# Optimization experiments

Hardware: AMD Instinct MI355X
Metric: run time of the kernel (lower is better)

The kernel has to match this reference:

```python
import jax, jax.numpy as jnp
import numpy as np

S = 3          # number of atomic species (experts)
N = 20000      # total atoms
F = 1920       # soap_size = S*(S+1)/2 * max_radial^2 * (max_angular+1) = 6*64*5
H = 512        # num_neurons_per_layer
NSTRUCT = 16   # number of structures (systems)
EPS = 1e-5


def setup_inputs() -> dict:
    key = jax.random.key(0)
    ks = jax.random.split(key, 12)
    std = 0.02
    return {
        "features": jax.random.normal(ks[0], (N, F), jnp.float32),
        "ln_gamma": jnp.ones((S, F), jnp.float32) + std * jax.random.normal(ks[1], (S, F), jnp.float32),
        "ln_beta": std * jax.random.normal(ks[2], (S, F), jnp.float32),
        "W1": std * jax.random.normal(ks[3], (S, F, H), jnp.float32),
        "b1": std * jax.random.normal(ks[4], (S, H), jnp.float32),
        "W2": std * jax.random.normal(ks[5], (S, H, H), jnp.float32),
        "b2": std * jax.random.normal(ks[6], (S, H), jnp.float32),
        "w3": std * jax.random.normal(ks[7], (S, H), jnp.float32),
        "b3": std * jax.random.normal(ks[8], (S,), jnp.float32),
        "comp_w": jax.random.normal(ks[9], (S,), jnp.float32),
        "species": jax.random.randint(ks[10], (N,), 0, S, dtype=jnp.int32),
        "struct_id": jax.random.randint(ks[11], (N,), 0, NSTRUCT, dtype=jnp.int32),
    }


def _silu(x):
    return x * jax.nn.sigmoid(x)


def reference(features, ln_gamma, ln_beta, W1, b1, W2, b2, w3, b3, comp_w, species, struct_id):
    # Per-species LayerNorm (LayerNormMap): normalization is species-independent,
    # only the affine params differ, so gather them per atom.
    mu = jnp.mean(features, axis=-1, keepdims=True)
    var = jnp.var(features, axis=-1, keepdims=True)
    xhat = (features - mu) * jax.lax.rsqrt(var + EPS)
    xln = xhat * ln_gamma[species] + ln_beta[species]  # [N, F]

    # Hard-routed per-species MLP (MLPMap) + per-species Linear->1 (LinearMap).
    # Small fixed loop over S experts; each atom keeps the output of its own expert.
    e = jnp.zeros((features.shape[0],), features.dtype)
    for s in range(S):
        h = _silu(xln @ W1[s] + b1[s])       # [N, H]
        h = _silu(h @ W2[s] + b2[s])         # [N, H]
        es = h @ w3[s] + b3[s]               # [N]
        e = jnp.where(species == s, es, e)

    # apply_composition_contribution: add per-species composition weight
    e = e + comp_w[species]

    # sum_over_samples(['atom','center_type']): per-structure energy
    energy = jax.ops.segment_sum(e, struct_id, num_segments=NSTRUCT)  # [NSTRUCT]
    return energy
```

## Files before the change

kernel.cpp:

```cpp
#include <hip/hip_runtime.h>
#include <cstdint>
#include <cstddef>

#define N_ATOMS 20000
#define F_DIM 1920
#define H_DIM 512
#define S_NUM 3
#define NSTRUCT_ 16
#define MAXT64 315
#define NCNT 8

#define QW 846.6667f
#define STEP_W (0.15f / 127.f)
#define QH 16.0f
#define STEP_H (1.f / 16.f)

typedef __bf16 bf16;
typedef float f32x4 __attribute__((ext_vector_type(4)));
typedef int i32x4 __attribute__((ext_vector_type(4)));

__device__ __forceinline__ void gload_lds16(const void* g, void* l) {
  __builtin_amdgcn_global_load_lds(
      (const __attribute__((address_space(1))) unsigned int*)g,
      (__attribute__((address_space(3))) unsigned int*)l, 16, 0, 0);
}

#define CNT8_OFF 16

__global__ __launch_bounds__(256) void prep_kernel(const float* __restrict__ W1,
                                                   int8_t* __restrict__ W1T,
                                                   const float* __restrict__ W2,
                                                   int8_t* __restrict__ W2T,
                                                   const int* __restrict__ species,
                                                   int* ints, float* out) {
  int id = blockIdx.x;
  if (id >= 912) {
    int cb = id - 912;
    int tid = threadIdx.x;
    if (cb == 0) {
      if (tid < 3) ints[tid] = 0;
      if (tid < NSTRUCT_) out[tid] = 0.f;
    }
    int base = cb * (N_ATOMS / NCNT);
    int end = base + (N_ATOMS / NCNT);
    int c0 = 0, c1 = 0, c2 = 0;
    for (int i = base + tid; i < end; i += 256) {
      int s = species[i];
      c0 += (s == 0);
      c1 += (s == 1);
      c2 += (s == 2);
    }
#pragma unroll
    for (int m = 1; m < 64; m <<= 1) {
      c0 += __shfl_xor(c0, m);
      c1 += __shfl_xor(c1, m);
      c2 += __shfl_xor(c2, m);
    }
    __shared__ int red[4][3];
    if ((tid & 63) == 0) {
      red[tid >> 6][0] = c0;
      red[tid >> 6][1] = c1;
      red[tid >> 6][2] = c2;
    }
    __syncthreads();
    if (tid == 0) {
      int* slot = ints + CNT8_OFF + cb * 3;
      slot[0] = red[0][0] + red[1][0] + red[2][0] + red[3][0];
      slot[1] = red[0][1] + red[1][1] + red[2][1] + red[3][1];
      slot[2] = red[0][2] + red[1][2] + red[2][2] + red[3][2];
    }
    return;
  }
  __shared__ float tile[64][65];
  const float* ins;
  int8_t* outs;
  int R, C, r0, c0;
  if (id < 720) {
    int sp = id / 240, rem = id % 240;
    R = F_DIM;
    C = H_DIM;
    c0 = (rem & 7) * 64;
    r0 = (rem >> 3) * 64;
    ins = W1 + (size_t)sp * R * C;
    outs = W1T + (size_t)sp * R * C;
  } else {
    int id2 = id - 720;
    int sp = id2 / 64, rem = id2 % 64;
    R = H_DIM;
    C = H_DIM;
    c0 = (rem & 7) * 64;
    r0 = (rem >> 3) * 64;
    ins = W2 + (size_t)sp * R * C;
    outs = W2T + (size_t)sp * R * C;
  }
  int tc = threadIdx.x & 63, tr4 = threadIdx.x >> 6;
#pragma unroll
  for (int it = 0; it < 16; ++it) {
    int r = it * 4 + tr4;
    tile[r][tc] = ins[(size_t)(r0 + r) * C + c0 + tc];
  }
  __syncthreads();
#pragma unroll
  for (int it = 0; it < 16; ++it) {
    int oc = it * 4 + tr4;
    float q = fminf(fmaxf(rintf(tile[tc][oc] * QW), -127.f), 127.f);
    outs[(size_t)(c0 + oc) * R + r0 + tc] = (int8_t)(int)q;
  }
}


__global__ void scatter_kernel(const int* __restrict__ species, int* ints,
                               int* idx_list, int* pos_of) {
  int n0 = 0, n1 = 0, n2 = 0;
#pragma unroll
  for (int b = 0; b < NCNT; ++b) {
    const int* slot = ints + CNT8_OFF + b * 3;
    n0 += slot[0];
    n1 += slot[1];
    n2 += slot[2];
  }
  int offs_l[4] = {0, n0, n0 + n1, N_ATOMS};
  if (blockIdx.x == 0 && threadIdx.x == 0) {
    int* offs = ints + 6;
    int* toffs = ints + 10;
    offs[0] = 0;
    offs[1] = n0;
    offs[2] = n0 + n1;
    offs[3] = N_ATOMS;
    int t0 = (n0 + 63) >> 6, t1 = (n1 + 63) >> 6, t2 = (n2 + 63) >> 6;
    toffs[0] = 0;
    toffs[1] = t0;
    toffs[2] = t0 + t1;
    toffs[3] = t0 + t1 + t2;
  }
  int* pos = ints;
  int i = blockIdx.x * 256 + threadIdx.x;
  int lane = threadIdx.x & 63;
  int sp = (i < N_ATOMS) ? species[i] : -1;
#pragma unroll
  for (int s = 0; s < S_NUM; ++s) {
    unsigned long long mask = __ballot(sp == s);
    if (!mask) continue;
    int leader = __ffsll((long long)mask) - 1;
    int base = 0;
    if (lane == leader) base = atomicAdd(&pos[s], __popcll(mask));
    base = __shfl(base, leader);
    if (sp == s) {
      int rank = __popcll(mask & ((1ULL << lane) - 1ULL));
      int p = offs_l[s] + base + rank;
      idx_list[p] = i;
      pos_of[i] = p;
    }
  }
}


__global__ __launch_bounds__(256) void ln_kernel(
    const float* __restrict__ feat, const float* __restrict__ gamma,
    const float* __restrict__ beta, const int* __restrict__ species,
    const int* __restrict__ pos_of, int8_t* __restrict__ xq,
    float* __restrict__ srowA) {
  int atom = blockIdx.x, tid = threadIdx.x;
  const float4* frow = (const float4*)(feat + (size_t)atom * F_DIM);
  float4 v0 = frow[tid];
  bool has2 = tid < 224;
  float4 v1 = has2 ? frow[256 + tid] : make_float4(0.f, 0.f, 0.f, 0.f);
  float s = v0.x + v0.y + v0.z + v0.w;
  float s2 = v0.x * v0.x + v0.y * v0.y + v0.z * v0.z + v0.w * v0.w;
  if (has2) {
    s += v1.x + v1.y + v1.z + v1.w;
    s2 += v1.x * v1.x + v1.y * v1.y + v1.z * v1.z + v1.w * v1.w;
  }
#pragma unroll
  for (int m = 1; m < 64; m <<= 1) {
    s += __shfl_xor(s, m);
    s2 += __shfl_xor(s2, m);
  }
  __shared__ float red[4][2];
  __shared__ float redm[4];
  if ((tid & 63) == 0) { red[tid >> 6][0] = s; red[tid >> 6][1] = s2; }
  __syncthreads();
  s = red[0][0] + red[1][0] + red[2][0] + red[3][0];
  s2 = red[0][1] + red[1][1] + red[2][1] + red[3][1];
  float mu = s * (1.f / F_DIM);
  float var = s2 * (1.f / F_DIM) - mu * mu;
  float rsig = rsqrtf(var + 1e-5f);
  int sp = species[atom];
  size_t p = (size_t)pos_of[atom];
  const float4* g4 = (const float4*)(gamma + (size_t)sp * F_DIM);
  const float4* b4 = (const float4*)(beta + (size_t)sp * F_DIM);
  float o0[4], o1[4];
  {
    float4 g = g4[tid], b = b4[tid];
    o0[0] = (v0.x - mu) * rsig * g.x + b.x;
    o0[1] = (v0.y - mu) * rsig * g.y + b.y;
    o0[2] = (v0.z - mu) * rsig * g.z + b.z;
    o0[3] = (v0.w - mu) * rsig * g.w + b.w;
  }
  if (has2) {
    float4 g = g4[256 + tid], b = b4[256 + tid];
    o1[0] = (v1.x - mu) * rsig * g.x + b.x;
    o1[1] = (v1.y - mu) * rsig * g.y + b.y;
    o1[2] = (v1.z - mu) * rsig * g.z + b.z;
    o1[3] = (v1.w - mu) * rsig * g.w + b.w;
  } else {
    o1[0] = o1[1] = o1[2] = o1[3] = 0.f;
  }
  float am = fmaxf(fmaxf(fabsf(o0[0]), fabsf(o0[1])), fmaxf(fabsf(o0[2]), fabsf(o0[3])));
  am = fmaxf(am, fmaxf(fmaxf(fabsf(o1[0]), fabsf(o1[1])), fmaxf(fabsf(o1[2]), fabsf(o1[3]))));
#pragma unroll
  for (int m = 1; m < 64; m <<= 1) am = fmaxf(am, __shfl_xor(am, m));
  if ((tid & 63) == 0) redm[tid >> 6] = am;
  __syncthreads();
  am = fmaxf(fmaxf(redm[0], redm[1]), fmaxf(redm[2], redm[3]));
  am = fmaxf(am, 1e-8f);
  float qs = 127.f / am;
  if (tid == 0) srowA[p] = am * (1.f / 127.f);
  unsigned int* orow = (unsigned int*)(xq + p * F_DIM);
  {
    int q0 = (int)rintf(o0[0] * qs), q1 = (int)rintf(o0[1] * qs);
    int q2 = (int)rintf(o0[2] * qs), q3 = (int)rintf(o0[3] * qs);
    orow[tid] = (q0 & 255) | ((q1 & 255) << 8) | ((q2 & 255) << 16) | ((q3 & 255) << 24);
  }
  if (has2) {
    int q0 = (int)rintf(o1[0] * qs), q1 = (int)rintf(o1[1] * qs);
    int q2 = (int)rintf(o1[2] * qs), q3 = (int)rintf(o1[3] * qs);
    orow[256 + tid] = (q0 & 255) | ((q1 & 255) << 8) | ((q2 & 255) << 16) | ((q3 & 255) << 24);
  }
}


template <int EPI>
__global__ __launch_bounds__(64, 2) void gemm_kernel(
    const int8_t* __restrict__ A, int lda_e, const int8_t* __restrict__ BT, int K,
    const float* __restrict__ bias, const float* __restrict__ w3,
    const float* __restrict__ srowA, int8_t* __restrict__ Hout,
    float* __restrict__ e_part, const int* __restrict__ ints) {
  __shared__ char smem[24576];
  const int* offs = ints + 6;
  const int* toffs = ints + 10;

  int total = gridDim.x;
  int lid = blockIdx.x;
  int q = total >> 3, r = total & 7;
  int xcd = lid & 7, sl = lid >> 3;
  int w = (xcd < r ? xcd * (q + 1) : r * (q + 1) + (xcd - r) * q) + sl;
  int bx = w & 3;
  int t = w >> 2;
  if (t >= toffs[3]) return;
  int sp = (t >= toffs[1]) + (t >= toffs[2]);
  int by = t - toffs[sp];

  int rstart = offs[sp], rend = offs[sp + 1];
  int r0 = rstart + by * 64;

  int lane = threadIdx.x;
  int n0 = bx * 128;

  const char* Ag = (const char*)A;
  size_t ldab = (size_t)lda_e;
  const char* Bg = (const char*)(BT + (size_t)sp * H_DIM * K);
  size_t ldbb = (size_t)K;

  int l8 = lane >> 3;
  int sw_st = (((lane & 7) ^ l8) << 4);

  auto stage = [&](int kt) {
    int k0b = kt * 128;
#pragma unroll
    for (int c = 0; c < 8; ++c) {
      int row = c * 8 + l8;
      int ar = r0 + row;
      if (ar > rend - 1) ar = rend - 1;
      gload_lds16(Ag + (size_t)ar * ldab + k0b + sw_st, &smem[c * 1024]);
    }
#pragma unroll
    for (int c = 0; c < 16; ++c) {
      int row = c * 8 + l8;
      gload_lds16(Bg + (size_t)(n0 + row) * ldbb + k0b + sw_st, &smem[8192 + c * 1024]);
    }
  };

  i32x4 acc[4][8];
#pragma unroll
  for (int a_ = 0; a_ < 4; ++a_)
#pragma unroll
    for (int b_ = 0; b_ < 8; ++b_) {
      i32x4 z = {0, 0, 0, 0};
      acc[a_][b_] = z;
    }

  int lr = lane & 15, lg = lane >> 4;
  int swr = (lr & 7) << 4;

  auto compute = [&]() {
#pragma unroll
    for (int kh = 0; kh < 2; ++kh) {
      int off = (kh * 64 + lg * 16) ^ swr;
      i32x4 av[4], bv[8];
#pragma unroll
      for (int fm = 0; fm < 4; ++fm)
        av[fm] = *(const i32x4*)(&smem[(fm * 16 + lr) * 128 + off]);
#pragma unroll
      for (int fn = 0; fn < 8; ++fn)
        bv[fn] = *(const i32x4*)(&smem[8192 + (fn * 16 + lr) * 128 + off]);
#pragma unroll
      for (int fm = 0; fm < 4; ++fm)
#pragma unroll
        for (int fn = 0; fn < 8; ++fn)
          acc[fm][fn] =
              __builtin_amdgcn_mfma_i32_16x16x64_i8(av[fm], bv[fn], acc[fm][fn], 0, 0, 0);
    }
  };

  int NT = K / 128;
#pragma unroll 1
  for (int kt = 0; kt < NT; ++kt) {
    stage(kt);
    __syncthreads();
    compute();
    __syncthreads();
  }

  const float* bs = bias + sp * H_DIM;
  if (EPI == 0) {
#pragma unroll
    for (int fm = 0; fm < 4; ++fm)
#pragma unroll
      for (int i = 0; i < 4; ++i) {
        int rr = r0 + fm * 16 + lg * 4 + i;
        if (rr < rend) {
          float deq = srowA[rr] * STEP_W;
#pragma unroll
          for (int fn = 0; fn < 8; ++fn) {
            int c = n0 + fn * 16 + lr;
            float x = (float)acc[fm][fn][i] * deq + bs[c];
            float h = x / (1.f + __expf(-x));
            float qh = fminf(fmaxf(rintf(h * QH), -127.f), 127.f);
            Hout[(size_t)rr * H_DIM + c] = (int8_t)(int)qh;
          }
        }
      }
  } else {
    const float* ws3 = w3 + sp * H_DIM;
    float* ep = e_part + (size_t)bx * N_ATOMS;
    const float deq = STEP_H * STEP_W;
#pragma unroll
    for (int fm = 0; fm < 4; ++fm)
#pragma unroll
      for (int i = 0; i < 4; ++i) {
        int rr = r0 + fm * 16 + lg * 4 + i;
        float part = 0.f;
#pragma unroll
        for (int fn = 0; fn < 8; ++fn) {
          int c = n0 + fn * 16 + lr;
          float x = (float)acc[fm][fn][i] * deq + bs[c];
          part += (x / (1.f + __expf(-x))) * ws3[c];
        }
        part += __shfl_xor(part, 1);
        part += __shfl_xor(part, 2);
        part += __shfl_xor(part, 4);
        part += __shfl_xor(part, 8);
        if (lr == 0 && rr < rend) ep[rr] = part;
      }
  }
}


__global__ void finalize_kernel(const float* __restrict__ e_part, const int* __restrict__ ints,
                                const float* __restrict__ b3, const float* __restrict__ comp_w,
                                const int* __restrict__ idx_list,
                                const int* __restrict__ struct_id, float* out) {
  const int* offs = ints + 6;
  __shared__ float bins[NSTRUCT_];
  if (threadIdx.x < NSTRUCT_) bins[threadIdx.x] = 0.f;
  __syncthreads();
  int rr = blockIdx.x * 256 + threadIdx.x;
  if (rr < N_ATOMS) {
    float e = 0.f;
#pragma unroll
    for (int p = 0; p < 4; ++p) e += e_part[(size_t)p * N_ATOMS + rr];
    int s = (rr >= offs[1]) + (rr >= offs[2]);
    e += b3[s] + comp_w[s];
    atomicAdd(&bins[struct_id[idx_list[rr]]], e);
  }
  __syncthreads();
  if (threadIdx.x < NSTRUCT_) atomicAdd(&out[threadIdx.x], bins[threadIdx.x]);
}


extern "C" void kernel_launch(void* const* d_in, const int* in_sizes, int n_in,
                              void* d_out, int out_size, void* d_ws, size_t ws_size,
                              hipStream_t stream) {
  const float* features = (const float*)d_in[0];
  const float* ln_gamma = (const float*)d_in[1];
  const float* ln_beta = (const float*)d_in[2];
  const float* W1 = (const float*)d_in[3];
  const float* b1 = (const float*)d_in[4];
  const float* W2 = (const float*)d_in[5];
  const float* b2 = (const float*)d_in[6];
  const float* w3 = (const float*)d_in[7];
  const float* b3 = (const float*)d_in[8];
  const float* comp_w = (const float*)d_in[9];
  const int* species = (const int*)d_in[10];
  const int* struct_id = (const int*)d_in[11];
  float* out = (float*)d_out;

  char* ws = (char*)d_ws;
  size_t off = 0;
  auto alloc = [&](size_t bytes) {
    char* p = ws + off;
    off += (bytes + 255) & ~(size_t)255;
    return p;
  };
  int8_t* W1T = (int8_t*)alloc((size_t)S_NUM * H_DIM * F_DIM);
  int8_t* W2T = (int8_t*)alloc((size_t)S_NUM * H_DIM * H_DIM);
  int8_t* xq = (int8_t*)alloc((size_t)N_ATOMS * F_DIM);
  int8_t* h1q = (int8_t*)alloc((size_t)N_ATOMS * H_DIM);
  float* srowA = (float*)alloc((size_t)N_ATOMS * 4);
  float* e_part = (float*)alloc((size_t)4 * N_ATOMS * 4);
  int* idx_list = (int*)alloc((size_t)N_ATOMS * 4);
  int* pos_of = (int*)alloc((size_t)N_ATOMS * 4);
  int* ints = (int*)alloc(256);

  int nb = (N_ATOMS + 255) / 256;
  prep_kernel<<<912 + NCNT, 256, 0, stream>>>(W1, W1T, W2, W2T, species, ints, out);
  scatter_kernel<<<nb, 256, 0, stream>>>(species, ints, idx_list, pos_of);
  ln_kernel<<<N_ATOMS, 256, 0, stream>>>(features, ln_gamma, ln_beta, species, pos_of, xq,
                                         srowA);

  gemm_kernel<0><<<4 * MAXT64, 64, 0, stream>>>(xq, F_DIM, W1T, F_DIM, b1, nullptr, srowA,
                                                h1q, nullptr, ints);
  gemm_kernel<1><<<4 * MAXT64, 64, 0, stream>>>(h1q, H_DIM, W2T, H_DIM, b2, w3, nullptr,
                                                nullptr, e_part, ints);
  finalize_kernel<<<nb, 256, 0, stream>>>(e_part, ints, b3, comp_w, idx_list, struct_id, out);
}
```

Before: 114.7 us.

## Fuse prep, scatter and layernorm into one kernel; gather rows in GEMM

Merges the weight transpose/quantize, the species counting/scatter, and the layernorm into a single launch. The scatter no longer relies on a global atomic counter: each block recomputes the species totals and its prefix over all atoms. The layernorm now writes rows in atom order, and the first GEMM gathers its A rows through idx_list. This removes two launches and the pos_of dependency. In exchange the scatter blocks do redundant full scans of species, and the first GEMM's A loads become indirect gathers.

```diff
diff --git a/kernel.cpp b/kernel.cpp
--- a/kernel.cpp
+++ b/kernel.cpp
@@ -8,7 +8,8 @@
 #define S_NUM 3
 #define NSTRUCT_ 16
 #define MAXT64 315
-#define NCNT 8
+#define NB_T 912
+#define NB_SC 79
 
 #define QW 846.6667f
 #define STEP_W (0.15f / 127.f)
@@ -25,142 +26,137 @@
       (__attribute__((address_space(3))) unsigned int*)l, 16, 0, 0);
 }
 
-#define CNT8_OFF 16
-
-__global__ __launch_bounds__(256) void prep_kernel(const float* __restrict__ W1,
-                                                   int8_t* __restrict__ W1T,
-                                                   const float* __restrict__ W2,
-                                                   int8_t* __restrict__ W2T,
-                                                   const int* __restrict__ species,
-                                                   int* ints, float* out) {
-  int id = blockIdx.x;
-  if (id >= 912) {
-    int cb = id - 912;
-    int tid = threadIdx.x;
-    if (cb == 0) {
-      if (tid < 3) ints[tid] = 0;
-      if (tid < NSTRUCT_) out[tid] = 0.f;
-    }
-    int base = cb * (N_ATOMS / NCNT);
-    int end = base + (N_ATOMS / NCNT);
-    int c0 = 0, c1 = 0, c2 = 0;
-    for (int i = base + tid; i < end; i += 256) {
-      int s = species[i];
-      c0 += (s == 0);
-      c1 += (s == 1);
-      c2 += (s == 2);
-    }
-#pragma unroll
-    for (int m = 1; m < 64; m <<= 1) {
-      c0 += __shfl_xor(c0, m);
-      c1 += __shfl_xor(c1, m);
-      c2 += __shfl_xor(c2, m);
-    }
-    __shared__ int red[4][3];
-    if ((tid & 63) == 0) {
-      red[tid >> 6][0] = c0;
-      red[tid >> 6][1] = c1;
-      red[tid >> 6][2] = c2;
-    }
-    __syncthreads();
-    if (tid == 0) {
-      int* slot = ints + CNT8_OFF + cb * 3;
-      slot[0] = red[0][0] + red[1][0] + red[2][0] + red[3][0];
-      slot[1] = red[0][1] + red[1][1] + red[2][1] + red[3][1];
-      slot[2] = red[0][2] + red[1][2] + red[2][2] + red[3][2];
-    }
-    return;
-  }
-  __shared__ float tile[64][65];
-  const float* ins;
-  int8_t* outs;
-  int R, C, r0, c0;
-  if (id < 720) {
-    int sp = id / 240, rem = id % 240;
-    R = F_DIM;
-    C = H_DIM;
-    c0 = (rem & 7) * 64;
-    r0 = (rem >> 3) * 64;
-    ins = W1 + (size_t)sp * R * C;
-    outs = W1T + (size_t)sp * R * C;
-  } else {
-    int id2 = id - 720;
-    int sp = id2 / 64, rem = id2 % 64;
-    R = H_DIM;
-    C = H_DIM;
-    c0 = (rem & 7) * 64;
-    r0 = (rem >> 3) * 64;
-    ins = W2 + (size_t)sp * R * C;
-    outs = W2T + (size_t)sp * R * C;
-  }
-  int tc = threadIdx.x & 63, tr4 = threadIdx.x >> 6;
-#pragma unroll
-  for (int it = 0; it < 16; ++it) {
-    int r = it * 4 + tr4;
-    tile[r][tc] = ins[(size_t)(r0 + r) * C + c0 + tc];
-  }
-  __syncthreads();
-#pragma unroll
-  for (int it = 0; it < 16; ++it) {
-    int oc = it * 4 + tr4;
-    float q = fminf(fmaxf(rintf(tile[tc][oc] * QW), -127.f), 127.f);
-    outs[(size_t)(c0 + oc) * R + r0 + tc] = (int8_t)(int)q;
-  }
-}
-
-
-__global__ void scatter_kernel(const int* __restrict__ species, int* ints,
-                               int* idx_list, int* pos_of) {
-  int n0 = 0, n1 = 0, n2 = 0;
-#pragma unroll
-  for (int b = 0; b < NCNT; ++b) {
-    const int* slot = ints + CNT8_OFF + b * 3;
-    n0 += slot[0];
-    n1 += slot[1];
-    n2 += slot[2];
-  }
-  int offs_l[4] = {0, n0, n0 + n1, N_ATOMS};
-  if (blockIdx.x == 0 && threadIdx.x == 0) {
-    int* offs = ints + 6;
-    int* toffs = ints + 10;
-    offs[0] = 0;
-    offs[1] = n0;
-    offs[2] = n0 + n1;
-    offs[3] = N_ATOMS;
-    int t0 = (n0 + 63) >> 6, t1 = (n1 + 63) >> 6, t2 = (n2 + 63) >> 6;
-    toffs[0] = 0;
-    toffs[1] = t0;
-    toffs[2] = t0 + t1;
-    toffs[3] = t0 + t1 + t2;
-  }
-  int* pos = ints;
-  int i = blockIdx.x * 256 + threadIdx.x;
-  int lane = threadIdx.x & 63;
-  int sp = (i < N_ATOMS) ? species[i] : -1;
-#pragma unroll
-  for (int s = 0; s < S_NUM; ++s) {
-    unsigned long long mask = __ballot(sp == s);
-    if (!mask) continue;
-    int leader = __ffsll((long long)mask) - 1;
-    int base = 0;
-    if (lane == leader) base = atomicAdd(&pos[s], __popcll(mask));
-    base = __shfl(base, leader);
-    if (sp == s) {
-      int rank = __popcll(mask & ((1ULL << lane) - 1ULL));
-      int p = offs_l[s] + base + rank;
-      idx_list[p] = i;
-      pos_of[i] = p;
-    }
-  }
-}
-
-
-__global__ __launch_bounds__(256) void ln_kernel(
+
+__global__ __launch_bounds__(256) void mega_kernel(
+    const float* __restrict__ W1, int8_t* __restrict__ W1T,
+    const float* __restrict__ W2, int8_t* __restrict__ W2T,
     const float* __restrict__ feat, const float* __restrict__ gamma,
     const float* __restrict__ beta, const int* __restrict__ species,
-    const int* __restrict__ pos_of, int8_t* __restrict__ xq,
-    float* __restrict__ srowA) {
-  int atom = blockIdx.x, tid = threadIdx.x;
+    int* ints, int* idx_list, int8_t* __restrict__ xq, float* __restrict__ srowA,
+    float* out) {
+  int id = blockIdx.x;
+  int tid = threadIdx.x;
+
+  if (id < NB_T) {
+    __shared__ float tile[64][65];
+    const float* ins;
+    int8_t* outs;
+    int R, C, r0, c0;
+    if (id < 720) {
+      int sp = id / 240, rem = id % 240;
+      R = F_DIM;
+      C = H_DIM;
+      c0 = (rem & 7) * 64;
+      r0 = (rem >> 3) * 64;
+      ins = W1 + (size_t)sp * R * C;
+      outs = W1T + (size_t)sp * R * C;
+    } else {
+      int id2 = id - 720;
+      int sp = id2 / 64, rem = id2 % 64;
+      R = H_DIM;
+      C = H_DIM;
+      c0 = (rem & 7) * 64;
+      r0 = (rem >> 3) * 64;
+      ins = W2 + (size_t)sp * R * C;
+      outs = W2T + (size_t)sp * R * C;
+    }
+    int tc = tid & 63, tr4 = tid >> 6;
+#pragma unroll
+    for (int it = 0; it < 16; ++it) {
+      int r = it * 4 + tr4;
+      tile[r][tc] = ins[(size_t)(r0 + r) * C + c0 + tc];
+    }
+    __syncthreads();
+#pragma unroll
+    for (int it = 0; it < 16; ++it) {
+      int oc = it * 4 + tr4;
+      float q = fminf(fmaxf(rintf(tile[tc][oc] * QW), -127.f), 127.f);
+      outs[(size_t)(c0 + oc) * R + r0 + tc] = (int8_t)(int)q;
+    }
+    return;
+  }
+
+  if (id < NB_T + NB_SC) {
+    int b = id - NB_T;
+    int base = b * 256;
+    if (b == 0 && tid < NSTRUCT_) out[tid] = 0.f;
+    int t0 = 0, t1 = 0, t2 = 0, p0 = 0, p1 = 0, p2 = 0;
+    for (int i = tid; i < N_ATOMS; i += 256) {
+      int s = species[i];
+      int b0 = (s == 0), b1 = (s == 1), b2 = (s == 2);
+      t0 += b0;
+      t1 += b1;
+      t2 += b2;
+      if (i < base) {
+        p0 += b0;
+        p1 += b1;
+        p2 += b2;
+      }
+    }
+#pragma unroll
+    for (int m = 1; m < 64; m <<= 1) {
+      t0 += __shfl_xor(t0, m);
+      t1 += __shfl_xor(t1, m);
+      t2 += __shfl_xor(t2, m);
+      p0 += __shfl_xor(p0, m);
+      p1 += __shfl_xor(p1, m);
+      p2 += __shfl_xor(p2, m);
+    }
+    __shared__ int red[4][6];
+    __shared__ int wcnt[4][3];
+    int wave = tid >> 6, lane = tid & 63;
+    if (lane == 0) {
+      red[wave][0] = t0;
+      red[wave][1] = t1;
+      red[wave][2] = t2;
+      red[wave][3] = p0;
+      red[wave][4] = p1;
+      red[wave][5] = p2;
+    }
+    __syncthreads();
+    t0 = red[0][0] + red[1][0] + red[2][0] + red[3][0];
+    t1 = red[0][1] + red[1][1] + red[2][1] + red[3][1];
+    t2 = red[0][2] + red[1][2] + red[2][2] + red[3][2];
+    p0 = red[0][3] + red[1][3] + red[2][3] + red[3][3];
+    p1 = red[0][4] + red[1][4] + red[2][4] + red[3][4];
+    p2 = red[0][5] + red[1][5] + red[2][5] + red[3][5];
+    if (b == 0 && tid == 0) {
+      int* offs = ints + 6;
+      int* toffs = ints + 10;
+      offs[0] = 0;
+      offs[1] = t0;
+      offs[2] = t0 + t1;
+      offs[3] = N_ATOMS;
+      int q0 = (t0 + 63) >> 6, q1 = (t1 + 63) >> 6, q2 = (t2 + 63) >> 6;
+      toffs[0] = 0;
+      toffs[1] = q0;
+      toffs[2] = q0 + q1;
+      toffs[3] = q0 + q1 + q2;
+    }
+    int i = base + tid;
+    int sp = (i < N_ATOMS) ? species[i] : -1;
+    unsigned long long m0 = __ballot(sp == 0);
+    unsigned long long m1 = __ballot(sp == 1);
+    unsigned long long m2 = __ballot(sp == 2);
+    if (lane == 0) {
+      wcnt[wave][0] = __popcll(m0);
+      wcnt[wave][1] = __popcll(m1);
+      wcnt[wave][2] = __popcll(m2);
+    }
+    __syncthreads();
+    if (sp >= 0) {
+      int offs_s = (sp == 0) ? 0 : (sp == 1 ? t0 : t0 + t1);
+      int pfx_s = (sp == 0) ? p0 : (sp == 1 ? p1 : p2);
+      unsigned long long msk = (sp == 0) ? m0 : (sp == 1 ? m1 : m2);
+      int rank = __popcll(msk & ((1ULL << lane) - 1ULL));
+      for (int w = 0; w < 4; ++w)
+        if (w < wave) rank += wcnt[w][sp];
+      idx_list[offs_s + pfx_s + rank] = i;
+    }
+    return;
+  }
+
+  int atom = id - (NB_T + NB_SC);
   const float4* frow = (const float4*)(feat + (size_t)atom * F_DIM);
   float4 v0 = frow[tid];
   bool has2 = tid < 224;
@@ -176,17 +172,16 @@
     s += __shfl_xor(s, m);
     s2 += __shfl_xor(s2, m);
   }
-  __shared__ float red[4][2];
+  __shared__ float redf[4][2];
   __shared__ float redm[4];
-  if ((tid & 63) == 0) { red[tid >> 6][0] = s; red[tid >> 6][1] = s2; }
+  if ((tid & 63) == 0) { redf[tid >> 6][0] = s; redf[tid >> 6][1] = s2; }
   __syncthreads();
-  s = red[0][0] + red[1][0] + red[2][0] + red[3][0];
-  s2 = red[0][1] + red[1][1] + red[2][1] + red[3][1];
+  s = redf[0][0] + redf[1][0] + redf[2][0] + redf[3][0];
+  s2 = redf[0][1] + redf[1][1] + redf[2][1] + redf[3][1];
   float mu = s * (1.f / F_DIM);
   float var = s2 * (1.f / F_DIM) - mu * mu;
   float rsig = rsqrtf(var + 1e-5f);
   int sp = species[atom];
-  size_t p = (size_t)pos_of[atom];
   const float4* g4 = (const float4*)(gamma + (size_t)sp * F_DIM);
   const float4* b4 = (const float4*)(beta + (size_t)sp * F_DIM);
   float o0[4], o1[4];
@@ -215,8 +210,8 @@
   am = fmaxf(fmaxf(redm[0], redm[1]), fmaxf(redm[2], redm[3]));
   am = fmaxf(am, 1e-8f);
   float qs = 127.f / am;
-  if (tid == 0) srowA[p] = am * (1.f / 127.f);
-  unsigned int* orow = (unsigned int*)(xq + p * F_DIM);
+  if (tid == 0) srowA[atom] = am * (1.f / 127.f);
+  unsigned int* orow = (unsigned int*)(xq + (size_t)atom * F_DIM);
   {
     int q0 = (int)rintf(o0[0] * qs), q1 = (int)rintf(o0[1] * qs);
     int q2 = (int)rintf(o0[2] * qs), q3 = (int)rintf(o0[3] * qs);
@@ -234,8 +229,9 @@
 __global__ __launch_bounds__(64, 2) void gemm_kernel(
     const int8_t* __restrict__ A, int lda_e, const int8_t* __restrict__ BT, int K,
     const float* __restrict__ bias, const float* __restrict__ w3,
-    const float* __restrict__ srowA, int8_t* __restrict__ Hout,
-    float* __restrict__ e_part, const int* __restrict__ ints) {
+    const float* __restrict__ srowA, const int* __restrict__ idx_list,
+    int8_t* __restrict__ Hout, float* __restrict__ e_part,
+    const int* __restrict__ ints) {
   __shared__ char smem[24576];
   const int* offs = ints + 6;
   const int* toffs = ints + 10;
@@ -265,15 +261,19 @@
   int l8 = lane >> 3;
   int sw_st = (((lane & 7) ^ l8) << 4);
 
+  int arow[8];
+#pragma unroll
+  for (int c = 0; c < 8; ++c) {
+    int rl = r0 + c * 8 + l8;
+    if (rl > rend - 1) rl = rend - 1;
+    arow[c] = (EPI == 0) ? idx_list[rl] : rl;
+  }
+
   auto stage = [&](int kt) {
     int k0b = kt * 128;
 #pragma unroll
-    for (int c = 0; c < 8; ++c) {
-      int row = c * 8 + l8;
-      int ar = r0 + row;
-      if (ar > rend - 1) ar = rend - 1;
-      gload_lds16(Ag + (size_t)ar * ldab + k0b + sw_st, &smem[c * 1024]);
-    }
+    for (int c = 0; c < 8; ++c)
+      gload_lds16(Ag + (size_t)arow[c] * ldab + k0b + sw_st, &smem[c * 1024]);
 #pragma unroll
     for (int c = 0; c < 16; ++c) {
       int row = c * 8 + l8;
@@ -330,7 +330,7 @@
       for (int i = 0; i < 4; ++i) {
         int rr = r0 + fm * 16 + lg * 4 + i;
         if (rr < rend) {
-          float deq = srowA[rr] * STEP_W;
+          float deq = srowA[idx_list[rr]] * STEP_W;
 #pragma unroll
           for (int fn = 0; fn < 8; ++fn) {
             int c = n0 + fn * 16 + lr;
@@ -420,18 +420,15 @@
   float* srowA = (float*)alloc((size_t)N_ATOMS * 4);
   float* e_part = (float*)alloc((size_t)4 * N_ATOMS * 4);
   int* idx_list = (int*)alloc((size_t)N_ATOMS * 4);
-  int* pos_of = (int*)alloc((size_t)N_ATOMS * 4);
   int* ints = (int*)alloc(256);
 
   int nb = (N_ATOMS + 255) / 256;
-  prep_kernel<<<912 + NCNT, 256, 0, stream>>>(W1, W1T, W2, W2T, species, ints, out);
-  scatter_kernel<<<nb, 256, 0, stream>>>(species, ints, idx_list, pos_of);
-  ln_kernel<<<N_ATOMS, 256, 0, stream>>>(features, ln_gamma, ln_beta, species, pos_of, xq,
-                                         srowA);
+  mega_kernel<<<NB_T + NB_SC + N_ATOMS, 256, 0, stream>>>(
+      W1, W1T, W2, W2T, features, ln_gamma, ln_beta, species, ints, idx_list, xq, srowA, out);
 
   gemm_kernel<0><<<4 * MAXT64, 64, 0, stream>>>(xq, F_DIM, W1T, F_DIM, b1, nullptr, srowA,
-                                                h1q, nullptr, ints);
+                                                idx_list, h1q, nullptr, ints);
   gemm_kernel<1><<<4 * MAXT64, 64, 0, stream>>>(h1q, H_DIM, W2T, H_DIM, b2, w3, nullptr,
-                                                nullptr, e_part, ints);
+                                                nullptr, nullptr, e_part, ints);
   finalize_kernel<<<nb, 256, 0, stream>>>(e_part, ints, b3, comp_w, idx_list, struct_id, out);
 }
```

After: 98.27 us, median of 2. -14.3%, faster.
